# Performance work log

Hardware: AMD Instinct MI355X
Metric: run time of the kernel (lower is better)

The kernel has to match this reference:

```python
import jax, jax.numpy as jnp
import numpy as np

EMBED_DIM = 768
NUM_HEADS = 12
HEAD_DIM = EMBED_DIM // NUM_HEADS
MLP_HIDDEN = int(EMBED_DIM * 4.0)
LN_EPS = 1e-5


def setup_inputs() -> dict:
    key = jax.random.key(0)
    ks = jax.random.split(key, 8)
    C, H = EMBED_DIM, MLP_HIDDEN
    s = 0.02
    return {
        "x": jax.random.normal(ks[0], (2, 2048, C), dtype=jnp.float32),
        "ln1_g": jnp.ones((C,), jnp.float32),
        "ln1_b": jnp.zeros((C,), jnp.float32),
        "qkv_w": jax.random.normal(ks[1], (3 * C, C), jnp.float32) * s,
        "proj_w": jax.random.normal(ks[2], (C, C), jnp.float32) * s,
        "proj_b": jnp.zeros((C,), jnp.float32),
        "ln2_g": jnp.ones((C,), jnp.float32),
        "ln2_b": jnp.zeros((C,), jnp.float32),
        "fc1_w": jax.random.normal(ks[3], (H, C), jnp.float32) * s,
        "fc1_b": jnp.zeros((H,), jnp.float32),
        "fc2_w": jax.random.normal(ks[4], (C, H), jnp.float32) * s,
        "fc2_b": jnp.zeros((C,), jnp.float32),
    }


def _layernorm(x, g, b):
    mu = jnp.mean(x, axis=-1, keepdims=True)
    var = jnp.mean(jnp.square(x - mu), axis=-1, keepdims=True)
    return (x - mu) * jax.lax.rsqrt(var + LN_EPS) * g + b


def reference(x, ln1_g, ln1_b, qkv_w, proj_w, proj_b, ln2_g, ln2_b,
              fc1_w, fc1_b, fc2_w, fc2_b):
    B, N, C = x.shape
    Hh, Dh = NUM_HEADS, HEAD_DIM
    scale = Dh ** -0.5

    # --- attention branch (pre-norm) ---
    h = _layernorm(x, ln1_g, ln1_b)
    qkv = h @ qkv_w.T                                   # [B,N,3C]
    qkv = qkv.reshape(B, N, 3, Hh, Dh)
    q = qkv[:, :, 0].transpose(0, 2, 1, 3)              # [B,H,N,D]
    k = qkv[:, :, 1].transpose(0, 2, 1, 3)
    v = qkv[:, :, 2].transpose(0, 2, 1, 3)
    attn = jnp.einsum('bhnd,bhmd->bhnm', q, k) * scale  # [B,H,N,N]
    attn = jax.nn.softmax(attn, axis=-1)
    o = jnp.einsum('bhnm,bhmd->bhnd', attn, v)          # [B,H,N,D]
    o = o.transpose(0, 2, 1, 3).reshape(B, N, C)
    x = x + o @ proj_w.T + proj_b

    # --- MLP branch (pre-norm), exact GELU like nn.GELU ---
    h = _layernorm(x, ln2_g, ln2_b)
    h = jax.nn.gelu(h @ fc1_w.T + fc1_b, approximate=False)
    x = x + h @ fc2_w.T + fc2_b
    return x
```

## Files before the change

kernel.cpp:

```cpp
#include <hip/hip_runtime.h>
#include <hip/hip_bf16.h>
#include <cstdint>
#include <math.h>


typedef __bf16 bf16_t;
typedef bf16_t bf16x4 __attribute__((ext_vector_type(4)));
typedef bf16_t bf16x8 __attribute__((ext_vector_type(8)));
typedef float floatx4 __attribute__((ext_vector_type(4)));

#define AS1 __attribute__((address_space(1)))
#define AS3 __attribute__((address_space(3)))

__device__ __forceinline__ void async_load16(const void* g, void* l) {
  const AS1 unsigned int* gp =
      reinterpret_cast<const AS1 unsigned int*>(reinterpret_cast<uintptr_t>(g));
  AS3 unsigned int* lp = reinterpret_cast<AS3 unsigned int*>(
      static_cast<unsigned int>(reinterpret_cast<uintptr_t>(l)));
  __builtin_amdgcn_global_load_lds(gp, lp, 16, 0, 0);
}

__device__ __forceinline__ bf16x8 lds_read8(const bf16_t* p) {
  return *reinterpret_cast<const bf16x8*>(p);
}

__global__ __launch_bounds__(256) void cvt_k(const float* __restrict__ in,
                                             bf16_t* __restrict__ out, int n4) {
  const int i = blockIdx.x * 256 + threadIdx.x;
  if (i < n4) {
    const float4 v = reinterpret_cast<const float4*>(in)[i];
    bf16x4 o;
    o[0] = (bf16_t)v.x; o[1] = (bf16_t)v.y; o[2] = (bf16_t)v.z; o[3] = (bf16_t)v.w;
    reinterpret_cast<bf16x4*>(out)[i] = o;
  }
}

__global__ __launch_bounds__(256) void cvt_all_k(
    const float* __restrict__ s0, const float* __restrict__ s1,
    const float* __restrict__ s2, const float* __restrict__ s3,
    bf16_t* __restrict__ d0, bf16_t* __restrict__ d1, bf16_t* __restrict__ d2,
    bf16_t* __restrict__ d3) {
  int i = blockIdx.x * 256 + threadIdx.x;
  const float* src;
  bf16_t* dst;
  if (i < 442368) { src = s0; dst = d0; }
  else if (i < 589824) { src = s1; dst = d1; i -= 442368; }
  else if (i < 1179648) { src = s2; dst = d2; i -= 589824; }
  else if (i < 1769472) { src = s3; dst = d3; i -= 1179648; }
  else return;
  const float4 v = reinterpret_cast<const float4*>(src)[i];
  bf16x4 o;
  o[0] = (bf16_t)v.x; o[1] = (bf16_t)v.y; o[2] = (bf16_t)v.z; o[3] = (bf16_t)v.w;
  reinterpret_cast<bf16x4*>(dst)[i] = o;
}

__global__ __launch_bounds__(256) void ln_k(const float* __restrict__ x,
                                            const float* __restrict__ g,
                                            const float* __restrict__ b,
                                            bf16_t* __restrict__ out) {
  const int row = blockIdx.x;
  const int tid = threadIdx.x;
  const float* xr = x + (long)row * 768;
  float v[3];
#pragma unroll
  for (int e = 0; e < 3; e++) v[e] = xr[tid + e * 256];
  float s = v[0] + v[1] + v[2];
  float ss = v[0] * v[0] + v[1] * v[1] + v[2] * v[2];
#pragma unroll
  for (int off = 32; off >= 1; off >>= 1) {
    s += __shfl_down(s, off, 64);
    ss += __shfl_down(ss, off, 64);
  }
  __shared__ float red[8];
  __shared__ float stat[2];
  const int wv = tid >> 6;
  if ((tid & 63) == 0) { red[wv] = s; red[4 + wv] = ss; }
  __syncthreads();
  if (tid == 0) {
    float S = red[0] + red[1] + red[2] + red[3];
    float SS = red[4] + red[5] + red[6] + red[7];
    float mu = S * (1.0f / 768.0f);
    float var = SS * (1.0f / 768.0f) - mu * mu;
    stat[0] = mu;
    stat[1] = rsqrtf(var + 1e-5f);
  }
  __syncthreads();
  const float mu = stat[0], rs = stat[1];
#pragma unroll
  for (int e = 0; e < 3; e++) {
    int c = tid + e * 256;
    out[(long)row * 768 + c] = (bf16_t)((v[e] - mu) * rs * g[c] + b[c]);
  }
}

template <int MODE>
__global__ __launch_bounds__(256, 2) void gemm_k(
    const bf16_t* __restrict__ A, const bf16_t* __restrict__ Bt, int lda,
    int ldb, int keff, int Nld, const float* __restrict__ bias,
    bf16_t* __restrict__ out_bf, bf16_t* __restrict__ q_out,
    bf16_t* __restrict__ k_out, bf16_t* __restrict__ vt_out) {
  constexpr int BK = 32;
  __shared__ __align__(16) bf16_t As[2][128 * BK];
  __shared__ __align__(16) bf16_t Bs[2][128 * BK];

  const int tid = threadIdx.x;
  const int w = tid >> 6;
  const int lane = tid & 63;
  const int quad = lane >> 4;
  const int lid = lane & 15;
  const int wr = (w >> 1) * 64;
  const int wc = (w & 1) * 64;
  const int mBase = blockIdx.y * 128;
  const int nBase = blockIdx.x * 128;

  const int ldsRowSub = lane >> 2;
  const int kblk = (lane & 3) ^ (ldsRowSub & 3);
  const int rq0 = (quad ^ (lid & 3)) * 8;
  const int c0 = w * 2, c1 = w * 2 + 1;
  const int rowA0 = c0 * 16 + ldsRowSub, rowA1 = c1 * 16 + ldsRowSub;

  const bf16_t* Ag = A + (long)mBase * lda;
  const bf16_t* Bg = Bt + (long)nBase * ldb;

  floatx4 acc[4][4];
#pragma unroll
  for (int i = 0; i < 4; i++)
#pragma unroll
    for (int j = 0; j < 4; j++) acc[i][j] = (floatx4){0.f, 0.f, 0.f, 0.f};

  async_load16(Ag + (long)rowA0 * lda + kblk * 8, &As[0][c0 * 512]);
  async_load16(Ag + (long)rowA1 * lda + kblk * 8, &As[0][c1 * 512]);
  async_load16(Bg + (long)rowA0 * ldb + kblk * 8, &Bs[0][c0 * 512]);
  async_load16(Bg + (long)rowA1 * ldb + kblk * 8, &Bs[0][c1 * 512]);

  const int iters = keff / BK;
  int cur = 0;
  for (int it = 0; it < iters; it++) {
    __syncthreads();
    if (it + 1 < iters) {
      const int k0 = (it + 1) * BK;
      const int nb = cur ^ 1;
      async_load16(Ag + (long)rowA0 * lda + k0 + kblk * 8, &As[nb][c0 * 512]);
      async_load16(Ag + (long)rowA1 * lda + k0 + kblk * 8, &As[nb][c1 * 512]);
      async_load16(Bg + (long)rowA0 * ldb + k0 + kblk * 8, &Bs[nb][c0 * 512]);
      async_load16(Bg + (long)rowA1 * ldb + k0 + kblk * 8, &Bs[nb][c1 * 512]);
    }

    bf16x8 af[4], bfv[4];
#pragma unroll
    for (int i = 0; i < 4; i++)
      af[i] = lds_read8(&As[cur][(wr + i * 16 + lid) * BK + rq0]);
#pragma unroll
    for (int j = 0; j < 4; j++)
      bfv[j] = lds_read8(&Bs[cur][(wc + j * 16 + lid) * BK + rq0]);
#pragma unroll
    for (int i = 0; i < 4; i++)
#pragma unroll
      for (int j = 0; j < 4; j++)
        acc[i][j] = __builtin_amdgcn_mfma_f32_16x16x32_bf16(af[i], bfv[j],
                                                            acc[i][j], 0, 0, 0);
    cur ^= 1;
  }

#pragma unroll
  for (int i = 0; i < 4; i++) {
    const int mRow = mBase + wr + i * 16 + quad * 4;
#pragma unroll
    for (int j = 0; j < 4; j++) {
      const int n = nBase + wc + j * 16 + lid;
      if constexpr (MODE == 0) {
        const int which = n / 768;
        const int rem = n - which * 768;
        const int head = rem >> 6;
        const int d = rem & 63;
        const int b = mRow >> 11;
        const int t = mRow & 2047;
        const int bh = b * 12 + head;
        if (which == 2) {
          bf16x4 pk;
#pragma unroll
          for (int r = 0; r < 4; r++) pk[r] = (bf16_t)acc[i][j][r];
          const long off = ((long)bh * 64 + d) * 2048 + t;
          *reinterpret_cast<bf16x4*>(&vt_out[off]) = pk;
        } else if (which == 0) {
#pragma unroll
          for (int r = 0; r < 4; r++)
            q_out[((long)bh * 2048 + t + r) * 64 + d] =
                (bf16_t)(acc[i][j][r] * 0.125f);
        } else {
#pragma unroll
          for (int r = 0; r < 4; r++)
            k_out[((long)bh * 2048 + t + r) * 64 + d] = (bf16_t)acc[i][j][r];
        }
      } else {
        const float bv = bias[n];
#pragma unroll
        for (int r = 0; r < 4; r++) {
          float v = acc[i][j][r] + bv;
          float ge = 0.5f * v * (1.0f + erff(v * 0.70710678118654752f));
          out_bf[(long)(mRow + r) * Nld + n] = (bf16_t)ge;
        }
      }
    }
  }
}

template <int MODE>
__global__ __launch_bounds__(256, 2) void gemm64_k(
    const bf16_t* __restrict__ A, const bf16_t* __restrict__ Bt, int lda,
    int ldb, int keff, int Nld, const float* __restrict__ bias,
    const float* __restrict__ resid_f, float* __restrict__ out_f) {
  constexpr int BK = 32;
  __shared__ __align__(16) bf16_t As[2][128 * BK];
  __shared__ __align__(16) bf16_t Bs[2][64 * BK];

  const int tid = threadIdx.x;
  const int w = tid >> 6;
  const int lane = tid & 63;
  const int quad = lane >> 4;
  const int lid = lane & 15;
  const int mBase = blockIdx.y * 128;
  const int nBase = blockIdx.x * 64;

  const int ldsRowSub = lane >> 2;
  const int kblk = (lane & 3) ^ (ldsRowSub & 3);
  const int rq0 = (quad ^ (lid & 3)) * 8;
  const int rowA0 = w * 16 + ldsRowSub;
  const int rowA1 = (w + 4) * 16 + ldsRowSub;

  const bf16_t* Ag = A + (long)mBase * lda;
  const bf16_t* Bg = Bt + (long)nBase * ldb;

  floatx4 acc[2][4];
#pragma unroll
  for (int i = 0; i < 2; i++)
#pragma unroll
    for (int j = 0; j < 4; j++) acc[i][j] = (floatx4){0.f, 0.f, 0.f, 0.f};

  async_load16(Ag + (long)rowA0 * lda + kblk * 8, &As[0][w * 512]);
  async_load16(Ag + (long)rowA1 * lda + kblk * 8, &As[0][(w + 4) * 512]);
  async_load16(Bg + (long)rowA0 * ldb + kblk * 8, &Bs[0][w * 512]);

  const int iters = keff / BK;
  int cur = 0;
  for (int it = 0; it < iters; it++) {
    __syncthreads();
    if (it + 1 < iters) {
      const int k0 = (it + 1) * BK;
      const int nb = cur ^ 1;
      async_load16(Ag + (long)rowA0 * lda + k0 + kblk * 8, &As[nb][w * 512]);
      async_load16(Ag + (long)rowA1 * lda + k0 + kblk * 8, &As[nb][(w + 4) * 512]);
      async_load16(Bg + (long)rowA0 * ldb + k0 + kblk * 8, &Bs[nb][w * 512]);
    }

    bf16x8 af[2], bfv[4];
#pragma unroll
    for (int i = 0; i < 2; i++)
      af[i] = lds_read8(&As[cur][(w * 32 + i * 16 + lid) * BK + rq0]);
#pragma unroll
    for (int j = 0; j < 4; j++)
      bfv[j] = lds_read8(&Bs[cur][(j * 16 + lid) * BK + rq0]);
#pragma unroll
    for (int i = 0; i < 2; i++)
#pragma unroll
      for (int j = 0; j < 4; j++)
        acc[i][j] = __builtin_amdgcn_mfma_f32_16x16x32_bf16(af[i], bfv[j],
                                                            acc[i][j], 0, 0, 0);
    cur ^= 1;
  }

#pragma unroll
  for (int i = 0; i < 2; i++) {
    const int mRow = mBase + w * 32 + i * 16 + quad * 4;
#pragma unroll
    for (int j = 0; j < 4; j++) {
      const int n = nBase + j * 16 + lid;
      if constexpr (MODE == 1) {
        const float bv = bias[n];
#pragma unroll
        for (int r = 0; r < 4; r++) {
          const long off = (long)(mRow + r) * Nld + n;
          out_f[off] = resid_f[off] + acc[i][j][r] + bv;
        }
      } else {
#pragma unroll
        for (int r = 0; r < 4; r++) {
          const long off = (long)(mRow + r) * Nld + n;
          out_f[off] += acc[i][j][r];
        }
      }
    }
  }
}

__global__ __launch_bounds__(512, 1) void flash_k(const bf16_t* __restrict__ q,
                                                  const bf16_t* __restrict__ kk,
                                                  const bf16_t* __restrict__ vt,
                                                  bf16_t* __restrict__ U,
                                                  float* __restrict__ lbuf) {
  constexpr int SK = 64, D = 64;
  __shared__ __align__(16) bf16_t Ks[2][SK * D];
  __shared__ __align__(16) bf16_t Vs[2][D * SK];

  const int tid = threadIdx.x;
  const int w = tid >> 6;
  const int lane = tid & 63;
  const int quad = lane >> 4;
  const int lid = lane & 15;
  const int bh = blockIdx.y;
  const int half = blockIdx.z;
  const int qBase = blockIdx.x * 128;

  const bf16_t* qg = q + ((long)bh * 2048 + qBase) * D;
  const bf16_t* kg = kk + ((long)bh * 2048 + half * 1024) * D;
  const bf16_t* vg = vt + (long)bh * D * 2048 + half * 1024;

  bf16x8 aq[2];
#pragma unroll
  for (int k2 = 0; k2 < 2; k2++)
    aq[k2] = *reinterpret_cast<const bf16x8*>(qg + (w * 16 + lid) * D +
                                              k2 * 32 + quad * 8);

  const int srow = lane >> 3;
  const int sdb = (lane & 7) ^ srow;
  const int rsw = lid & 7;

  async_load16(kg + (long)(w * 8 + srow) * D + sdb * 8, &Ks[0][w * 512]);
  async_load16(vg + (long)(w * 8 + srow) * 2048 + sdb * 8, &Vs[0][w * 512]);

  float lsum = 0.f;
  floatx4 oacc[4];
#pragma unroll
  for (int jo = 0; jo < 4; jo++) oacc[jo] = (floatx4){0.f, 0.f, 0.f, 0.f};

  int cur = 0;
  for (int kci = 0; kci < 16; kci++) {
    __syncthreads();
    if (kci + 1 < 16) {
      const int kc = (kci + 1) * 64;
      const int nb = cur ^ 1;
      async_load16(kg + (long)(kc + w * 8 + srow) * D + sdb * 8, &Ks[nb][w * 512]);
      async_load16(vg + (long)(w * 8 + srow) * 2048 + kc + sdb * 8, &Vs[nb][w * 512]);
    }

    floatx4 sacc[4];
#pragma unroll
    for (int jm = 0; jm < 4; jm++) sacc[jm] = (floatx4){0.f, 0.f, 0.f, 0.f};
#pragma unroll
    for (int k2 = 0; k2 < 2; k2++) {
#pragma unroll
      for (int jm = 0; jm < 4; jm++) {
        const bf16x8 ak = lds_read8(
            &Ks[cur][(jm * 16 + lid) * D + (((k2 * 4 + quad) ^ rsw) * 8)]);
        sacc[jm] =
            __builtin_amdgcn_mfma_f32_16x16x32_bf16(ak, aq[k2], sacc[jm], 0, 0, 0);
      }
    }

    bf16x8 ap[2];
#pragma unroll
    for (int k2 = 0; k2 < 2; k2++) {
      uint32_t pk[2][2];
#pragma unroll
      for (int j = 0; j < 2; j++) {
        const int jm = k2 * 2 + j;
        const float p0 = exp2f(fmaf(sacc[jm][0], 1.44269504f, -11.5415603f));
        const float p1 = exp2f(fmaf(sacc[jm][1], 1.44269504f, -11.5415603f));
        const float p2 = exp2f(fmaf(sacc[jm][2], 1.44269504f, -11.5415603f));
        const float p3 = exp2f(fmaf(sacc[jm][3], 1.44269504f, -11.5415603f));
        lsum += ((p0 + p1) + p2) + p3;
        asm("v_cvt_pk_bf16_f32 %0, %1, %2" : "=v"(pk[j][0]) : "v"(p0), "v"(p1));
        asm("v_cvt_pk_bf16_f32 %0, %1, %2" : "=v"(pk[j][1]) : "v"(p2), "v"(p3));
      }
      asm("v_permlane32_swap_b32 %0, %1" : "+v"(pk[0][0]), "+v"(pk[1][0]));
      asm("v_permlane16_swap_b32 %0, %1" : "+v"(pk[0][0]), "+v"(pk[1][0]));
      asm("v_permlane32_swap_b32 %0, %1" : "+v"(pk[0][1]), "+v"(pk[1][1]));
      asm("v_permlane16_swap_b32 %0, %1" : "+v"(pk[0][1]), "+v"(pk[1][1]));
      union { uint32_t u[4]; bf16x8 v; } au;
      au.u[0] = pk[0][0];
      au.u[1] = pk[0][1];
      au.u[2] = pk[1][0];
      au.u[3] = pk[1][1];
      ap[k2] = au.v;
    }

#pragma unroll
    for (int k2 = 0; k2 < 2; k2++) {
#pragma unroll
      for (int jo = 0; jo < 4; jo++) {
        const bf16x8 bv = lds_read8(
            &Vs[cur][(jo * 16 + lid) * SK + (((k2 * 4 + quad) ^ rsw) * 8)]);
        oacc[jo] =
            __builtin_amdgcn_mfma_f32_16x16x32_bf16(ap[k2], bv, oacc[jo], 0, 0, 0);
      }
    }
    cur ^= 1;
  }

  lsum += __shfl_xor(lsum, 16, 64);
  lsum += __shfl_xor(lsum, 32, 64);

  const long lrow = ((long)half * 24 + bh) * 2048 + qBase + w * 16;
  if (quad == 0) lbuf[lrow + lid] = lsum;

  bf16_t* Ub = U + (((long)half * 24 + bh) * 2048 + qBase) * D;
#pragma unroll
  for (int jo = 0; jo < 4; jo++) {
#pragma unroll
    for (int r = 0; r < 4; r++) {
      const int t = w * 16 + quad * 4 + r;
      Ub[(long)t * D + jo * 16 + lid] = (bf16_t)oacc[jo][r];
    }
  }
}

__global__ __launch_bounds__(256) void combine_k(const bf16_t* __restrict__ U,
                                                 const float* __restrict__ lbuf,
                                                 bf16_t* __restrict__ o) {
  const int idx = blockIdx.x * 256 + threadIdx.x;
  const int bh = idx >> 17;
  const int rem = idx & 131071;
  const int t = rem >> 6;
  const int d = rem & 63;
  const float l0 = lbuf[bh * 2048 + t];
  const float l1 = lbuf[(24 + bh) * 2048 + t];
  const float u = (float)U[idx] + (float)U[3145728 + idx];
  const int b = bh / 12;
  const int head = bh - b * 12;
  o[((long)b * 2048 + t) * 768 + head * 64 + d] = (bf16_t)(u / (l0 + l1));
}

extern "C" void kernel_launch(void* const* d_in, const int* in_sizes, int n_in,
                              void* d_out, int out_size, void* d_ws,
                              size_t ws_size, hipStream_t stream) {
  (void)in_sizes; (void)n_in; (void)out_size;
  const float* x = (const float*)d_in[0];
  const float* ln1_g = (const float*)d_in[1];
  const float* ln1_b = (const float*)d_in[2];
  const float* qkv_w = (const float*)d_in[3];
  const float* proj_w = (const float*)d_in[4];
  const float* proj_b = (const float*)d_in[5];
  const float* ln2_g = (const float*)d_in[6];
  const float* ln2_b = (const float*)d_in[7];
  const float* fc1_w = (const float*)d_in[8];
  const float* fc1_b = (const float*)d_in[9];
  const float* fc2_w = (const float*)d_in[10];
  const float* fc2_b = (const float*)d_in[11];
  float* out = (float*)d_out;
  char* ws = (char*)d_ws;

  const bool big = ws_size >= (size_t)64487424;

  if (big) {
    bf16_t* wqkv = (bf16_t*)(ws + 0);
    bf16_t* wproj = (bf16_t*)(ws + 3538944);
    bf16_t* wfc1 = (bf16_t*)(ws + 4718592);
    bf16_t* wfc2 = (bf16_t*)(ws + 9437184);
    bf16_t* h1 = (bf16_t*)(ws + 14155776);
    bf16_t* ob = h1;
    bf16_t* qb = (bf16_t*)(ws + 20447232);
    bf16_t* kb = (bf16_t*)(ws + 26738688);
    bf16_t* vtb = (bf16_t*)(ws + 33030144);
    bf16_t* Ubuf = (bf16_t*)(ws + 39321600);
    float* lbuf = (float*)(ws + 51904512);
    float* x1 = (float*)(ws + 20447232);
    bf16_t* h2 = (bf16_t*)(ws + 33030144);
    bf16_t* hg = (bf16_t*)(ws + 39321600);

    cvt_all_k<<<6912, 256, 0, stream>>>(qkv_w, proj_w, fc1_w, fc2_w, wqkv,
                                        wproj, wfc1, wfc2);
    ln_k<<<4096, 256, 0, stream>>>(x, ln1_g, ln1_b, h1);
    gemm_k<0><<<dim3(18, 32), 256, 0, stream>>>(h1, wqkv, 768, 768, 768, 2304,
                                                nullptr, nullptr, qb, kb, vtb);
    flash_k<<<dim3(16, 24, 2), 512, 0, stream>>>(qb, kb, vtb, Ubuf, lbuf);
    combine_k<<<12288, 256, 0, stream>>>(Ubuf, lbuf, ob);
    gemm64_k<1><<<dim3(12, 32), 256, 0, stream>>>(ob, wproj, 768, 768, 768, 768,
                                                  proj_b, x, x1);
    ln_k<<<4096, 256, 0, stream>>>(x1, ln2_g, ln2_b, h2);
    gemm_k<2><<<dim3(24, 32), 256, 0, stream>>>(h2, wfc1, 768, 768, 768, 3072,
                                                fc1_b, hg, nullptr, nullptr,
                                                nullptr);
    gemm64_k<1><<<dim3(12, 32), 256, 0, stream>>>(hg, wfc2, 3072, 3072, 3072,
                                                  768, fc2_b, x1, out);
  } else {
    bf16_t* wqkv = (bf16_t*)(ws + 0);
    bf16_t* wproj = (bf16_t*)(ws + 3538944);
    bf16_t* h1 = (bf16_t*)(ws + 4718592);
    bf16_t* ob = h1;
    bf16_t* qb = (bf16_t*)(ws + 11010048);
    bf16_t* kb = (bf16_t*)(ws + 17301504);
    bf16_t* vtb = (bf16_t*)(ws + 23592960);
    float* x1 = (float*)(ws + 11010048);
    bf16_t* h2 = (bf16_t*)(ws + 23592960);
    bf16_t* wfc1 = (bf16_t*)(ws + 0);
    bf16_t* wfc2 = (bf16_t*)(ws + 4718592);
    bf16_t* hg = (bf16_t*)(ws + 29884416);
    bf16_t* Ubuf = (bf16_t*)(ws + 29884416);
    float* lbuf = (float*)(ws + 42467328);

    cvt_k<<<1728, 256, 0, stream>>>(qkv_w, wqkv, 442368);
    cvt_k<<<576, 256, 0, stream>>>(proj_w, wproj, 147456);
    ln_k<<<4096, 256, 0, stream>>>(x, ln1_g, ln1_b, h1);
    gemm_k<0><<<dim3(18, 32), 256, 0, stream>>>(h1, wqkv, 768, 768, 768, 2304,
                                                nullptr, nullptr, qb, kb, vtb);
    flash_k<<<dim3(16, 24, 2), 512, 0, stream>>>(qb, kb, vtb, Ubuf, lbuf);
    combine_k<<<12288, 256, 0, stream>>>(Ubuf, lbuf, ob);
    gemm64_k<1><<<dim3(12, 32), 256, 0, stream>>>(ob, wproj, 768, 768, 768, 768,
                                                  proj_b, x, x1);
    cvt_k<<<2304, 256, 0, stream>>>(fc1_w, wfc1, 589824);
    cvt_k<<<2304, 256, 0, stream>>>(fc2_w, wfc2, 589824);
    ln_k<<<4096, 256, 0, stream>>>(x1, ln2_g, ln2_b, h2);
    for (int h = 0; h < 2; h++) {
      gemm_k<2><<<dim3(12, 32), 256, 0, stream>>>(
          h2, wfc1 + (long)h * 1536 * 768, 768, 768, 768, 1536,
          fc1_b + h * 1536, hg, nullptr, nullptr, nullptr);
      if (h == 0)
        gemm64_k<1><<<dim3(12, 32), 256, 0, stream>>>(hg, wfc2 + 0, 1536, 3072,
                                                      1536, 768, fc2_b, x1, out);
      else
        gemm64_k<5><<<dim3(12, 32), 256, 0, stream>>>(hg, wfc2 + 1536, 1536,
                                                      3072, 1536, 768, nullptr,
                                                      nullptr, out);
    }
  }
}
```

Measured before the change: 286.0 us.

## Split-K the fc2 GEMM with atomic accumulation, init output in LayerNorm

The second LayerNorm kernel now also writes x1 + fc2_b into the output buffer. The fc2 GEMM becomes a split-K launch over two K halves that atomically add their partial sums into that buffer. This doubles the number of blocks for the 768-wide output, which only had 384 blocks before, and removes the residual read from the GEMM epilogue. It also raises the gemm64 occupancy hint to 4 blocks per SM. The cost is float atomic traffic, summation order that now varies between runs, and extra register pressure from the launch-bounds change.

```diff
diff --git a/kernel.cpp b/kernel.cpp
--- a/kernel.cpp
+++ b/kernel.cpp
@@ -54,10 +54,13 @@
   reinterpret_cast<bf16x4*>(dst)[i] = o;
 }
 
+template <int INIT>
 __global__ __launch_bounds__(256) void ln_k(const float* __restrict__ x,
                                             const float* __restrict__ g,
                                             const float* __restrict__ b,
-                                            bf16_t* __restrict__ out) {
+                                            bf16_t* __restrict__ out,
+                                            const float* __restrict__ b2,
+                                            float* __restrict__ oinit) {
   const int row = blockIdx.x;
   const int tid = threadIdx.x;
   const float* xr = x + (long)row * 768;
@@ -90,6 +93,7 @@
   for (int e = 0; e < 3; e++) {
     int c = tid + e * 256;
     out[(long)row * 768 + c] = (bf16_t)((v[e] - mu) * rs * g[c] + b[c]);
+    if constexpr (INIT == 1) oinit[(long)row * 768 + c] = v[e] + b2[c];
   }
 }
 
@@ -206,7 +210,7 @@
 }
 
 template <int MODE>
-__global__ __launch_bounds__(256, 2) void gemm64_k(
+__global__ __launch_bounds__(256, 4) void gemm64_k(
     const bf16_t* __restrict__ A, const bf16_t* __restrict__ Bt, int lda,
     int ldb, int keff, int Nld, const float* __restrict__ bias,
     const float* __restrict__ resid_f, float* __restrict__ out_f) {
@@ -221,6 +225,7 @@
   const int lid = lane & 15;
   const int mBase = blockIdx.y * 128;
   const int nBase = blockIdx.x * 64;
+  const int kOff = blockIdx.z * keff;
 
   const int ldsRowSub = lane >> 2;
   const int kblk = (lane & 3) ^ (ldsRowSub & 3);
@@ -228,8 +233,8 @@
   const int rowA0 = w * 16 + ldsRowSub;
   const int rowA1 = (w + 4) * 16 + ldsRowSub;
 
-  const bf16_t* Ag = A + (long)mBase * lda;
-  const bf16_t* Bg = Bt + (long)nBase * ldb;
+  const bf16_t* Ag = A + (long)mBase * lda + kOff;
+  const bf16_t* Bg = Bt + (long)nBase * ldb + kOff;
 
   floatx4 acc[2][4];
 #pragma unroll
@@ -286,7 +291,7 @@
 #pragma unroll
         for (int r = 0; r < 4; r++) {
           const long off = (long)(mRow + r) * Nld + n;
-          out_f[off] += acc[i][j][r];
+          unsafeAtomicAdd(&out_f[off], acc[i][j][r]);
         }
       }
     }
@@ -469,19 +474,19 @@
 
     cvt_all_k<<<6912, 256, 0, stream>>>(qkv_w, proj_w, fc1_w, fc2_w, wqkv,
                                         wproj, wfc1, wfc2);
-    ln_k<<<4096, 256, 0, stream>>>(x, ln1_g, ln1_b, h1);
+    ln_k<0><<<4096, 256, 0, stream>>>(x, ln1_g, ln1_b, h1, nullptr, nullptr);
     gemm_k<0><<<dim3(18, 32), 256, 0, stream>>>(h1, wqkv, 768, 768, 768, 2304,
                                                 nullptr, nullptr, qb, kb, vtb);
     flash_k<<<dim3(16, 24, 2), 512, 0, stream>>>(qb, kb, vtb, Ubuf, lbuf);
     combine_k<<<12288, 256, 0, stream>>>(Ubuf, lbuf, ob);
     gemm64_k<1><<<dim3(12, 32), 256, 0, stream>>>(ob, wproj, 768, 768, 768, 768,
                                                   proj_b, x, x1);
-    ln_k<<<4096, 256, 0, stream>>>(x1, ln2_g, ln2_b, h2);
+    ln_k<1><<<4096, 256, 0, stream>>>(x1, ln2_g, ln2_b, h2, fc2_b, out);
     gemm_k<2><<<dim3(24, 32), 256, 0, stream>>>(h2, wfc1, 768, 768, 768, 3072,
                                                 fc1_b, hg, nullptr, nullptr,
                                                 nullptr);
-    gemm64_k<1><<<dim3(12, 32), 256, 0, stream>>>(hg, wfc2, 3072, 3072, 3072,
-                                                  768, fc2_b, x1, out);
+    gemm64_k<6><<<dim3(12, 32, 2), 256, 0, stream>>>(hg, wfc2, 3072, 3072, 1536,
+                                                     768, nullptr, nullptr, out);
   } else {
     bf16_t* wqkv = (bf16_t*)(ws + 0);
     bf16_t* wproj = (bf16_t*)(ws + 3538944);
@@ -500,7 +505,7 @@
 
     cvt_k<<<1728, 256, 0, stream>>>(qkv_w, wqkv, 442368);
     cvt_k<<<576, 256, 0, stream>>>(proj_w, wproj, 147456);
-    ln_k<<<4096, 256, 0, stream>>>(x, ln1_g, ln1_b, h1);
+    ln_k<0><<<4096, 256, 0, stream>>>(x, ln1_g, ln1_b, h1, nullptr, nullptr);
     gemm_k<0><<<dim3(18, 32), 256, 0, stream>>>(h1, wqkv, 768, 768, 768, 2304,
                                                 nullptr, nullptr, qb, kb, vtb);
     flash_k<<<dim3(16, 24, 2), 512, 0, stream>>>(qb, kb, vtb, Ubuf, lbuf);
@@ -509,18 +514,14 @@
                                                   proj_b, x, x1);
     cvt_k<<<2304, 256, 0, stream>>>(fc1_w, wfc1, 589824);
     cvt_k<<<2304, 256, 0, stream>>>(fc2_w, wfc2, 589824);
-    ln_k<<<4096, 256, 0, stream>>>(x1, ln2_g, ln2_b, h2);
+    ln_k<1><<<4096, 256, 0, stream>>>(x1, ln2_g, ln2_b, h2, fc2_b, out);
     for (int h = 0; h < 2; h++) {
       gemm_k<2><<<dim3(12, 32), 256, 0, stream>>>(
           h2, wfc1 + (long)h * 1536 * 768, 768, 768, 768, 1536,
           fc1_b + h * 1536, hg, nullptr, nullptr, nullptr);
-      if (h == 0)
-        gemm64_k<1><<<dim3(12, 32), 256, 0, stream>>>(hg, wfc2 + 0, 1536, 3072,
-                                                      1536, 768, fc2_b, x1, out);
-      else
-        gemm64_k<5><<<dim3(12, 32), 256, 0, stream>>>(hg, wfc2 + 1536, 1536,
-                                                      3072, 1536, 768, nullptr,
-                                                      nullptr, out);
-    }
-  }
-}
+      gemm64_k<6><<<dim3(12, 32), 256, 0, stream>>>(hg, wfc2 + h * 1536, 1536,
+                                                    3072, 1536, 768, nullptr,
+                                                    nullptr, out);
+    }
+  }
+}
```

After: 295.2 us. 3.2% more time.
